# Optimization experiments

Measured on AMD Instinct MI355X. Metric: run time of the kernel, lower is better.

The kernel has to match this reference:

```python
import jax, jax.numpy as jnp
import numpy as np

EPS = 1e-8
VOX_WIDTH = 1.0
CURV_THRESH = 0.5


def _build_kernels():
    """Nine 3x3x3 central finite-difference stencils, pre-divided by vox_width / vox_width^2."""
    def zk():
        return np.zeros((3, 3, 3), np.float32)
    ks = {}
    # first derivatives (central difference), denominator vox_width
    for name, ax in (('ddx', 0), ('ddy', 1), ('ddz', 2)):
        k = zk(); i = [1, 1, 1]
        i[ax] = 0; k[tuple(i)] = -0.5
        i[ax] = 2; k[tuple(i)] = 0.5
        ks[name] = k / VOX_WIDTH
    # pure second derivatives, denominator vox_width^2
    for name, ax in (('d2dx2', 0), ('d2dy2', 1), ('d2dz2', 2)):
        k = zk(); i = [1, 1, 1]
        i[ax] = 0; k[tuple(i)] = 1.0
        i[ax] = 1; k[tuple(i)] = -2.0
        i[ax] = 2; k[tuple(i)] = 1.0
        ks[name] = k / VOX_WIDTH ** 2
    # mixed second derivatives, denominator vox_width^2
    for name, (a, b) in (('d2dxdy', (0, 1)), ('d2dxdz', (0, 2)), ('d2dydz', (1, 2))):
        k = zk()
        for sa, sb, v in ((0, 0, 0.25), (0, 2, -0.25), (2, 0, -0.25), (2, 2, 0.25)):
            i = [1, 1, 1]; i[a] = sa; i[b] = sb; k[tuple(i)] = v
        ks[name] = k / VOX_WIDTH ** 2
    order = ['ddx', 'ddy', 'ddz', 'd2dx2', 'd2dy2', 'd2dz2', 'd2dxdy', 'd2dxdz', 'd2dydz']
    return np.stack([ks[n] for n in order])[:, None]  # [9, 1, 3, 3, 3]


_KERNELS = jnp.asarray(_build_kernels())


def setup_inputs() -> dict:
    key = jax.random.key(0)
    phi = jax.random.normal(key, (2, 1, 192, 192, 192), dtype=jnp.float32)
    return {"phi": phi}


def reference(phi):
    # all nine stencils as one valid 3D conv: [N, 9, D-2, H-2, W-2]
    g = jax.lax.conv_general_dilated(
        phi, _KERNELS, window_strides=(1, 1, 1), padding='VALID',
        dimension_numbers=('NCDHW', 'OIDHW', 'NCDHW'))
    gx, gy, gz, hxx, hyy, hzz, hxy, hxz, hyz = (g[:, i:i + 1] for i in range(9))

    mag = jnp.sqrt(gx * gx + gy * gy + gz * gz + EPS)
    mag3 = mag ** 3

    # mean curvature: sum_{i!=j} g_i^2 H_jj - 2 sum_{i<j} g_i g_j H_ij, over |grad|^3
    cross = gx * gy * hxy + gx * gz * hxz + gy * gz * hyz
    mean_c = (gx * gx * (hyy + hzz) + gy * gy * (hxx + hzz) + gz * gz * (hxx + hyy)
              - 2.0 * cross) / (mag3 + EPS)

    # gaussian curvature: laplacian/|grad| - (g^T H g)/|grad|^3
    lap = (hxx + hyy + hzz) / (mag + EPS)
    quad = (gx * gx * hxx + gy * gy * hyy + gz * gz * hzz + 2.0 * cross) / (mag3 + EPS)
    gauss = lap - quad

    k1 = mean_c + jnp.sqrt(jnp.abs(mean_c ** 2 - gauss) + EPS)
    pen = jax.nn.relu((k1 / (CURV_THRESH + EPS)) ** 2 - 1.0)

    # zero crossings of phi over 3x3x3 neighborhoods (valid -> matches conv output shape)
    mn = jax.lax.reduce_window(phi, jnp.inf, jax.lax.min, (1, 1, 3, 3, 3), (1, 1, 1, 1, 1), 'VALID')
    mx = jax.lax.reduce_window(phi, -jnp.inf, jax.lax.max, (1, 1, 3, 3, 3), (1, 1, 1, 1, 1), 'VALID')
    phi_zero = jax.lax.stop_gradient((mn * mx < 0).astype(phi.dtype))

    return jnp.sum(phi_zero * pen) / (jnp.sum(phi_zero) + EPS)
```

## Files before the change

### kernel.cpp

```cpp
#include <hip/hip_runtime.h>


typedef float v2f __attribute__((ext_vector_type(2)));

constexpr int DIM  = 192;
constexpr int ODIM = 190;
constexpr int TX = 32, TY = 32, CZ = 19;
constexpr int NTX = 6, NTY = 6, NTZ = 10;
constexpr int PLANE = DIM * DIM;
constexpr int NBLOCKS = 2 * NTZ * NTY * NTX;

struct Slice {
    v2f   q[3][4];
    float xmn[4], xmx[4];
};

__global__ __launch_bounds__(256, 3) void curv_main(const float* __restrict__ phi,
                                                    double* __restrict__ acc,
                                                    int use_partials) {
    int bx = blockIdx.x;
    const int tx = bx % NTX; bx /= NTX;
    const int ty = bx % NTY; bx /= NTY;
    const int tz = bx % NTZ; bx /= NTZ;
    const int n  = bx;

    const int xbase = tx * TX, ybase = ty * TY, zbase = tz * CZ;
    const int tid = threadIdx.x;
    const int row = tid >> 3;
    const int x0  = (tid & 7) * 4;
    const float* pn = phi + (long long)n * DIM * PLANE;

    const int c4 = xbase + x0;
    int c2t = c4 + 4; if (c2t > DIM - 2) c2t = DIM - 2;
    const int c2 = c2t;
    int yoff[3];
#pragma unroll
    for (int dy = 0; dy < 3; ++dy) {
        int iy = ybase + row + dy; if (iy > DIM - 1) iy = DIM - 1;
        yoff[dy] = iy * DIM;
    }

    float4 t4[3]; float2 t2[3];
    auto pref = [&](int g) {
        const float* base = pn + (zbase + g) * PLANE;
#pragma unroll
        for (int dy = 0; dy < 3; ++dy) {
            t4[dy] = *(const float4*)(base + yoff[dy] + c4);
            t2[dy] = *(const float2*)(base + yoff[dy] + c2);
        }
    };

    auto unpack = [&](Slice& s) {
        float mn6[6], mx6[6];
#pragma unroll
        for (int dy = 0; dy < 3; ++dy) {
            const float4 a = t4[dy]; const float2 b = t2[dy];
            s.q[dy][0] = (v2f){a.x, a.z};
            s.q[dy][1] = (v2f){a.y, a.w};
            s.q[dy][2] = (v2f){a.z, b.x};
            s.q[dy][3] = (v2f){a.w, b.y};
            if (dy == 0) {
                mn6[0] = a.x; mn6[1] = a.y; mn6[2] = a.z;
                mn6[3] = a.w; mn6[4] = b.x; mn6[5] = b.y;
                mx6[0] = a.x; mx6[1] = a.y; mx6[2] = a.z;
                mx6[3] = a.w; mx6[4] = b.x; mx6[5] = b.y;
            } else {
                mn6[0] = fminf(mn6[0], a.x); mx6[0] = fmaxf(mx6[0], a.x);
                mn6[1] = fminf(mn6[1], a.y); mx6[1] = fmaxf(mx6[1], a.y);
                mn6[2] = fminf(mn6[2], a.z); mx6[2] = fmaxf(mx6[2], a.z);
                mn6[3] = fminf(mn6[3], a.w); mx6[3] = fmaxf(mx6[3], a.w);
                mn6[4] = fminf(mn6[4], b.x); mx6[4] = fmaxf(mx6[4], b.x);
                mn6[5] = fminf(mn6[5], b.y); mx6[5] = fmaxf(mx6[5], b.y);
            }
        }
#pragma unroll
        for (int j = 0; j < 4; ++j) {
            s.xmn[j] = fminf(fminf(mn6[j], mn6[j + 1]), mn6[j + 2]);
            s.xmx[j] = fmaxf(fmaxf(mx6[j], mx6[j + 1]), mx6[j + 2]);
        }
    };

    float fsp = 0.0f, fsc = 0.0f;
    const float EPSF = 1e-8f;
    const float EPS4 = 4e-8f;
    const int oy = ybase + row;

    bool vmask[4];
#pragma unroll
    for (int j = 0; j < 4; ++j)
        vmask[j] = (oy < ODIM) && (xbase + x0 + j < ODIM);

    auto compute = [&](const Slice& s0, const Slice& s1, const Slice& s2) {
        float wmn[4], wmx[4];
#pragma unroll
        for (int j = 0; j < 4; ++j) {
            wmn[j] = fminf(fminf(s0.xmn[j], s1.xmn[j]), s2.xmn[j]);
            wmx[j] = fmaxf(fmaxf(s0.xmx[j], s1.xmx[j]), s2.xmx[j]);
        }

#pragma unroll
        for (int p = 0; p < 2; ++p) {
            v2f Gx = s2.q[1][p + 1] - s0.q[1][p + 1];
            v2f Gy = s1.q[2][p + 1] - s1.q[0][p + 1];
            v2f Gz = s1.q[1][p + 2] - s1.q[1][p];

            v2f c2v = 2.0f * s1.q[1][p + 1];
            v2f hxx = s0.q[1][p + 1] - c2v + s2.q[1][p + 1];
            v2f hyy = s1.q[0][p + 1] - c2v + s1.q[2][p + 1];
            v2f hzz = s1.q[1][p] - c2v + s1.q[1][p + 2];

            v2f Mxy = s0.q[0][p + 1] - s0.q[2][p + 1]
                    - s2.q[0][p + 1] + s2.q[2][p + 1];
            v2f Mxz = s0.q[1][p] - s0.q[1][p + 2]
                    - s2.q[1][p] + s2.q[1][p + 2];
            v2f Myz = s1.q[0][p] - s1.q[0][p + 2]
                    - s1.q[2][p] + s1.q[2][p + 2];

            v2f Gx2 = Gx * Gx, Gy2 = Gy * Gy, Gz2 = Gz * Gz;
            v2f mag2G = Gx2 + Gy2 + Gz2 + EPS4;

            v2f r = (v2f){ __builtin_amdgcn_rsqf(mag2G.x),
                           __builtin_amdgcn_rsqf(mag2G.y) };
            v2f r3 = r * r * r;
            v2f twor3 = r3 + r3;

            v2f crossG = Gx * Gy * Mxy + Gx * Gz * Mxz + Gy * Gz * Myz;

            v2f num1 = Gx2 * (hyy + hzz) + Gy2 * (hxx + hzz) +
                       Gz2 * (hxx + hyy) - 0.5f * crossG;
            v2f mean_c = num1 * twor3;
            v2f lap   = (hxx + hyy + hzz) * (r + r);
            v2f num2  = Gx2 * hxx + Gy2 * hyy + Gz2 * hzz + 0.5f * crossG;
            v2f quad  = num2 * twor3;
            v2f gauss = lap - quad;

            v2f disc = mean_c * mean_c - gauss;
            v2f sq = (v2f){ sqrtf(fabsf(disc.x) + EPSF),
                            sqrtf(fabsf(disc.y) + EPSF) };
            v2f k1 = mean_c + sq;
            v2f t  = 2.0f * k1;
            v2f pen2 = t * t - 1.0f;

#pragma unroll
            for (int e = 0; e < 2; ++e) {
                const int j = p + 2 * e;
                float pen = fmaxf(e ? pen2.y : pen2.x, 0.0f);
                if (vmask[j] && (wmn[j] * wmx[j] < 0.0f)) {
                    fsp += pen;
                    fsc += 1.0f;
                }
            }
        }
    };

    Slice s0, s1, s2;

    pref(0); unpack(s0);
    pref(1); unpack(s1);
    pref(2);

    unpack(s2); pref(3);  compute(s0, s1, s2);
    unpack(s0); pref(4);  compute(s1, s2, s0);
    unpack(s1); pref(5);  compute(s2, s0, s1);
    unpack(s2); pref(6);  compute(s0, s1, s2);
    unpack(s0); pref(7);  compute(s1, s2, s0);
    unpack(s1); pref(8);  compute(s2, s0, s1);
    unpack(s2); pref(9);  compute(s0, s1, s2);
    unpack(s0); pref(10); compute(s1, s2, s0);
    unpack(s1); pref(11); compute(s2, s0, s1);
    unpack(s2); pref(12); compute(s0, s1, s2);
    unpack(s0); pref(13); compute(s1, s2, s0);
    unpack(s1); pref(14); compute(s2, s0, s1);
    unpack(s2); pref(15); compute(s0, s1, s2);
    unpack(s0); pref(16); compute(s1, s2, s0);
    unpack(s1); pref(17); compute(s2, s0, s1);
    unpack(s2); pref(18); compute(s0, s1, s2);
    unpack(s0); pref(19); compute(s1, s2, s0);
    unpack(s1); pref(20); compute(s2, s0, s1);
    unpack(s2);           compute(s0, s1, s2);

    double sp = (double)fsp, sc = (double)fsc;
#pragma unroll
    for (int off = 32; off > 0; off >>= 1) {
        sp += __shfl_down(sp, off, 64);
        sc += __shfl_down(sc, off, 64);
    }

    __shared__ double lsp[4], lsc[4];
    const int wave = tid >> 6, lane = tid & 63;
    if (lane == 0) { lsp[wave] = sp; lsc[wave] = sc; }
    __syncthreads();
    if (tid == 0) {
        double tp = lsp[0] + lsp[1] + lsp[2] + lsp[3];
        double tc = lsc[0] + lsc[1] + lsc[2] + lsc[3];
        if (use_partials) {
            acc[2 * blockIdx.x]     = tp;
            acc[2 * blockIdx.x + 1] = tc;
        } else {
            atomicAdd(&acc[0], tp);
            atomicAdd(&acc[1], tc);
        }
    }
}

__global__ __launch_bounds__(256) void curv_reduce(const double* __restrict__ part,
                                                   int nblocks, int use_partials,
                                                   float* __restrict__ out) {
    double sp = 0.0, sc = 0.0;
    if (use_partials) {
        for (int i = threadIdx.x; i < nblocks; i += 256) {
            sp += part[2 * i];
            sc += part[2 * i + 1];
        }
    } else if (threadIdx.x == 0) {
        sp = part[0]; sc = part[1];
    }
#pragma unroll
    for (int off = 32; off > 0; off >>= 1) {
        sp += __shfl_down(sp, off, 64);
        sc += __shfl_down(sc, off, 64);
    }
    __shared__ double lsp[4], lsc[4];
    const int wave = threadIdx.x >> 6, lane = threadIdx.x & 63;
    if (lane == 0) { lsp[wave] = sp; lsc[wave] = sc; }
    __syncthreads();
    if (threadIdx.x == 0) {
        double tp = lsp[0] + lsp[1] + lsp[2] + lsp[3];
        double tc = lsc[0] + lsc[1] + lsc[2] + lsc[3];
        out[0] = (float)(tp / (tc + 1e-8));
    }
}

extern "C" void kernel_launch(void* const* d_in, const int* in_sizes, int n_in,
                              void* d_out, int out_size, void* d_ws, size_t ws_size,
                              hipStream_t stream) {
    const float* phi = (const float*)d_in[0];
    float* out = (float*)d_out;
    double* acc = (double*)d_ws;

    const int use_partials = (ws_size >= (size_t)(2 * NBLOCKS) * sizeof(double)) ? 1 : 0;
    if (!use_partials) {
        hipMemsetAsync(d_ws, 0, 2 * sizeof(double), stream);
    }

    curv_main<<<NBLOCKS, 256, 0, stream>>>(phi, acc, use_partials);
    curv_reduce<<<1, 256, 0, stream>>>(acc, NBLOCKS, use_partials, out);
}
```

Baseline: 105.7 us.

## Deepen z-slab to 30 planes with double-buffered two-ahead prefetch loop

Result: slower. 110.8 us (+4.9%).

```diff
diff --git a/kernel.cpp b/kernel.cpp
--- a/kernel.cpp
+++ b/kernel.cpp
@@ -5,8 +5,8 @@
 
 constexpr int DIM  = 192;
 constexpr int ODIM = 190;
-constexpr int TX = 32, TY = 32, CZ = 19;
-constexpr int NTX = 6, NTY = 6, NTZ = 10;
+constexpr int TX = 32, TY = 32, CZ = 30;
+constexpr int NTX = 6, NTY = 6, NTZ = 7;
 constexpr int PLANE = DIM * DIM;
 constexpr int NBLOCKS = 2 * NTZ * NTY * NTX;
 
@@ -15,7 +15,7 @@
     float xmn[4], xmx[4];
 };
 
-__global__ __launch_bounds__(256, 3) void curv_main(const float* __restrict__ phi,
+__global__ __launch_bounds__(256, 2) void curv_main(const float* __restrict__ phi,
                                                     double* __restrict__ acc,
                                                     int use_partials) {
     int bx = blockIdx.x;
@@ -40,17 +40,27 @@
         yoff[dy] = iy * DIM;
     }
 
-    float4 t4[3]; float2 t2[3];
-    auto pref = [&](int g) {
-        const float* base = pn + (zbase + g) * PLANE;
+    float4 t4a[3], t4b[3]; float2 t2a[3], t2b[3];
+    auto prefA = [&](int g) {
+        int gz = zbase + g; if (gz > DIM - 1) gz = DIM - 1;
+        const float* base = pn + gz * PLANE;
 #pragma unroll
         for (int dy = 0; dy < 3; ++dy) {
-            t4[dy] = *(const float4*)(base + yoff[dy] + c4);
-            t2[dy] = *(const float2*)(base + yoff[dy] + c2);
-        }
-    };
-
-    auto unpack = [&](Slice& s) {
+            t4a[dy] = *(const float4*)(base + yoff[dy] + c4);
+            t2a[dy] = *(const float2*)(base + yoff[dy] + c2);
+        }
+    };
+    auto prefB = [&](int g) {
+        int gz = zbase + g; if (gz > DIM - 1) gz = DIM - 1;
+        const float* base = pn + gz * PLANE;
+#pragma unroll
+        for (int dy = 0; dy < 3; ++dy) {
+            t4b[dy] = *(const float4*)(base + yoff[dy] + c4);
+            t2b[dy] = *(const float2*)(base + yoff[dy] + c2);
+        }
+    };
+
+    auto unpack_from = [&](const float4* t4, const float2* t2, Slice& s) {
         float mn6[6], mx6[6];
 #pragma unroll
         for (int dy = 0; dy < 3; ++dy) {
@@ -79,6 +89,8 @@
             s.xmx[j] = fmaxf(fmaxf(mx6[j], mx6[j + 1]), mx6[j + 2]);
         }
     };
+    auto unpackA = [&](Slice& s) { unpack_from(t4a, t2a, s); };
+    auto unpackB = [&](Slice& s) { unpack_from(t4b, t2b, s); };
 
     float fsp = 0.0f, fsc = 0.0f;
     const float EPSF = 1e-8f;
@@ -90,7 +102,10 @@
     for (int j = 0; j < 4; ++j)
         vmask[j] = (oy < ODIM) && (xbase + x0 + j < ODIM);
 
-    auto compute = [&](const Slice& s0, const Slice& s1, const Slice& s2) {
+    auto compute = [&](const Slice& s0, const Slice& s1, const Slice& s2, int zo) {
+        const int oz = zbase + zo;
+        if (oz >= ODIM) return;
+
         float wmn[4], wmx[4];
 #pragma unroll
         for (int j = 0; j < 4; ++j) {
@@ -125,12 +140,13 @@
             v2f twor3 = r3 + r3;
 
             v2f crossG = Gx * Gy * Mxy + Gx * Gz * Mxz + Gy * Gz * Myz;
+            v2f ch = 0.5f * crossG;
 
             v2f num1 = Gx2 * (hyy + hzz) + Gy2 * (hxx + hzz) +
-                       Gz2 * (hxx + hyy) - 0.5f * crossG;
+                       Gz2 * (hxx + hyy) - ch;
             v2f mean_c = num1 * twor3;
             v2f lap   = (hxx + hyy + hzz) * (r + r);
-            v2f num2  = Gx2 * hxx + Gy2 * hyy + Gz2 * hzz + 0.5f * crossG;
+            v2f num2  = Gx2 * hxx + Gy2 * hyy + Gz2 * hzz + ch;
             v2f quad  = num2 * twor3;
             v2f gauss = lap - quad;
 
@@ -155,29 +171,19 @@
 
     Slice s0, s1, s2;
 
-    pref(0); unpack(s0);
-    pref(1); unpack(s1);
-    pref(2);
-
-    unpack(s2); pref(3);  compute(s0, s1, s2);
-    unpack(s0); pref(4);  compute(s1, s2, s0);
-    unpack(s1); pref(5);  compute(s2, s0, s1);
-    unpack(s2); pref(6);  compute(s0, s1, s2);
-    unpack(s0); pref(7);  compute(s1, s2, s0);
-    unpack(s1); pref(8);  compute(s2, s0, s1);
-    unpack(s2); pref(9);  compute(s0, s1, s2);
-    unpack(s0); pref(10); compute(s1, s2, s0);
-    unpack(s1); pref(11); compute(s2, s0, s1);
-    unpack(s2); pref(12); compute(s0, s1, s2);
-    unpack(s0); pref(13); compute(s1, s2, s0);
-    unpack(s1); pref(14); compute(s2, s0, s1);
-    unpack(s2); pref(15); compute(s0, s1, s2);
-    unpack(s0); pref(16); compute(s1, s2, s0);
-    unpack(s1); pref(17); compute(s2, s0, s1);
-    unpack(s2); pref(18); compute(s0, s1, s2);
-    unpack(s0); pref(19); compute(s1, s2, s0);
-    unpack(s1); pref(20); compute(s2, s0, s1);
-    unpack(s2);           compute(s0, s1, s2);
+    prefA(0); prefB(1);
+    unpackA(s0);
+    unpackB(s1);
+    prefA(2); prefB(3);
+
+    for (int z = 0; z < CZ; z += 6) {
+        unpackA(s2); prefA(z + 4);  compute(s0, s1, s2, z);
+        unpackB(s0); prefB(z + 5);  compute(s1, s2, s0, z + 1);
+        unpackA(s1); prefA(z + 6);  compute(s2, s0, s1, z + 2);
+        unpackB(s2); prefB(z + 7);  compute(s0, s1, s2, z + 3);
+        unpackA(s0); prefA(z + 8);  compute(s1, s2, s0, z + 4);
+        unpackB(s1); prefB(z + 9);  compute(s2, s0, s1, z + 5);
+    }
 
     double sp = (double)fsp, sc = (double)fsc;
 #pragma unroll
```
